# Kernel tuning notes

Hardware: AMD Instinct MI355X
Metric: run time of the kernel (lower is better)

Reference implementation:

```python
import jax, jax.numpy as jnp
import numpy as np

B, D, E, T, P = 65536, 256, 256, 128, 8  # batch, memory_dim, edge_feat_dim, time_dim, num_prototypes
LN_EPS = 1e-6
NORM_EPS = 1e-6


def _layer_norm(x, w, b):
    mu = jnp.mean(x, axis=-1, keepdims=True)
    var = jnp.mean(jnp.square(x - mu), axis=-1, keepdims=True)
    return (x - mu) / jnp.sqrt(var + LN_EPS) * w + b


def setup_inputs() -> dict:
    key = jax.random.key(0)
    ks = jax.random.split(key, 10)
    qin = D + E + T            # query_proj in_features
    gin = 2 * D + T            # gate_proj in_features
    return {
        "raw_memory": jax.random.normal(ks[0], (B, D), dtype=jnp.float32),
        "node_features": jax.random.normal(ks[1], (B, D), dtype=jnp.float32),
        "edge_features": jax.random.normal(ks[2], (B, E), dtype=jnp.float32),
        "time_encoding": jax.random.normal(ks[3], (B, T), dtype=jnp.float32),
        "prototypes": jax.random.normal(ks[4], (B, P, D), dtype=jnp.float32),
        # learned params (xavier gain=0.1 -> small)
        "Wq": jax.random.normal(ks[5], (D, qin), dtype=jnp.float32) * (0.1 * np.sqrt(2.0 / (D + qin))),
        "bq": jnp.zeros((D,), dtype=jnp.float32),
        "Wg": jax.random.normal(ks[6], (1, gin), dtype=jnp.float32) * (0.1 * np.sqrt(2.0 / (1 + gin))),
        "bg": jnp.zeros((1,), dtype=jnp.float32),
        "temperature": jnp.ones((1,), dtype=jnp.float32),
        "ln_w": jnp.ones((D,), dtype=jnp.float32),
        "ln_b": jnp.zeros((D,), dtype=jnp.float32),
    }


def reference(raw_memory, node_features, edge_features, time_encoding, prototypes,
              Wq, bq, Wg, bg, temperature, ln_w, ln_b):
    # query projection (inputs are finite so _sanitize_tensor is identity)
    q_in = jnp.concatenate([raw_memory, edge_features, time_encoding], axis=-1)  # [B, D+E+T]
    query = jnp.tanh(_layer_norm(q_in @ Wq.T + bq, ln_w, ln_b))                   # [B, D]

    # cosine similarity to per-node prototypes (F.normalize uses max(norm, eps))
    qn = query / jnp.maximum(jnp.linalg.norm(query, axis=-1, keepdims=True), NORM_EPS)
    pn = prototypes / jnp.maximum(jnp.linalg.norm(prototypes, axis=-1, keepdims=True), NORM_EPS)
    sim = jnp.clip(jnp.einsum('bd,bpd->bp', qn, pn), -10.0, 10.0)                 # [B, P]
    temp = jnp.clip(temperature, 0.5, 5.0)
    sim = sim / (temp + 0.01)

    attn = jnp.clip(jax.nn.softmax(sim, axis=-1), 0.0, 1.0)                       # [B, P]
    candidate = jnp.clip(jnp.einsum('bp,bpd->bd', attn, prototypes), -5.0, 5.0)   # [B, D]

    # gated update
    g_in = jnp.clip(jnp.concatenate([raw_memory, candidate, time_encoding], axis=-1), -50.0, 50.0)
    gate = jax.nn.sigmoid(jnp.clip(g_in @ Wg.T + bg, -10.0, 10.0))                # [B, 1]
    updated = (1.0 - gate) * raw_memory + gate * candidate
    updated = jnp.clip(_layer_norm(updated, ln_w, ln_b), -10.0, 10.0)
    return updated
```

## Files before the change

kernel.cpp:

```cpp
#include <hip/hip_runtime.h>
#include <cstdint>
#include <cstddef>

#define D 256
#define E 256
#define T 128
#define QIN 640
#define P 8
#define R 16
#define KP 648
#define DP 260

typedef __attribute__((ext_vector_type(8))) short bf16x8;
typedef __attribute__((ext_vector_type(4))) float f32x4;

__device__ __forceinline__ ushort f2bf(float f) {
  uint32_t u = __float_as_uint(f);
  u += 0x7fffu + ((u >> 16) & 1u);
  return (ushort)(u >> 16);
}

__device__ __forceinline__ float wsum(float v) {
#pragma unroll
  for (int o = 32; o > 0; o >>= 1) v += __shfl_xor(v, o, 64);
  return v;
}

__device__ __forceinline__ void wsum2(float& a, float& b) {
#pragma unroll
  for (int o = 32; o > 0; o >>= 1) {
    a += __shfl_xor(a, o, 64);
    b += __shfl_xor(b, o, 64);
  }
}

__device__ __forceinline__ float clampf(float x, float lo, float hi) {
  return fminf(fmaxf(x, lo), hi);
}

__global__ void prep_w2_kernel(const float* __restrict__ Wq, ushort* __restrict__ W2) {
  const int idx = blockIdx.x * 256 + threadIdx.x;
  const int n = idx / QIN;
  const int k = idx - n * QIN;
  W2[((((k >> 3) * D + n) << 3)) + (k & 7)] = f2bf(Wq[idx]);
}

template <bool PRE>
__global__ __launch_bounds__(256, 4) void fused_kernel(
    const float* __restrict__ raw, const float* __restrict__ edge,
    const float* __restrict__ tim, const float* __restrict__ proto,
    const float* __restrict__ Wq, const ushort* __restrict__ W2,
    const float* __restrict__ bq, const float* __restrict__ Wg,
    const float* __restrict__ bg, const float* __restrict__ temp,
    const float* __restrict__ lnw, const float* __restrict__ lnb,
    float* __restrict__ out) {
  __shared__ ushort qa[R][KP];
  __shared__ float qpre[R][DP];

  const int tid = threadIdx.x;
  const int r0 = blockIdx.x * R;

#pragma unroll
  for (int it = 0; it < (R * QIN / 4) / 256; ++it) {
    const int flat = it * 256 + tid;
    const int r = flat / (QIN / 4);
    const int p4 = (flat - r * (QIN / 4)) * 4;
    const size_t g = (size_t)(r0 + r);
    float4 v;
    if (p4 < D)          v = *(const float4*)(raw + g * D + p4);
    else if (p4 < D + E) v = *(const float4*)(edge + g * E + (p4 - D));
    else                 v = *(const float4*)(tim + g * T + (p4 - D - E));
    ushort4 h;
    h.x = f2bf(v.x); h.y = f2bf(v.y); h.z = f2bf(v.z); h.w = f2bf(v.w);
    *(ushort4*)&qa[r][p4] = h;
  }
  __syncthreads();

  const int w = tid >> 6;
  const int lane = tid & 63;
  const int lr = lane & 15;
  const int lh = lane >> 4;

  {
    f32x4 acc[4];
#pragma unroll
    for (int c = 0; c < 4; ++c) acc[c] = (f32x4){0.f, 0.f, 0.f, 0.f};

    for (int kb = 0; kb < QIN; kb += 32) {
      const bf16x8 af = *(const bf16x8*)&qa[lr][kb + lh * 8];
#pragma unroll
      for (int c = 0; c < 4; ++c) {
        const int n = w * 64 + c * 16 + lr;
        bf16x8 bfv;
        if (PRE) {
          bfv = *(const bf16x8*)&W2[(((kb >> 3) + lh) * D + n) << 3];
        } else {
          const float* src = Wq + (size_t)n * QIN + kb + lh * 8;
          const float4 a0 = *(const float4*)src;
          const float4 a1 = *(const float4*)(src + 4);
          bfv[0] = (short)f2bf(a0.x); bfv[1] = (short)f2bf(a0.y);
          bfv[2] = (short)f2bf(a0.z); bfv[3] = (short)f2bf(a0.w);
          bfv[4] = (short)f2bf(a1.x); bfv[5] = (short)f2bf(a1.y);
          bfv[6] = (short)f2bf(a1.z); bfv[7] = (short)f2bf(a1.w);
        }
        acc[c] = __builtin_amdgcn_mfma_f32_16x16x32_bf16(af, bfv, acc[c], 0, 0, 0);
      }
    }

#pragma unroll
    for (int c = 0; c < 4; ++c) {
      const int n = w * 64 + c * 16 + lr;
      const float bqv = bq[n];
#pragma unroll
      for (int i = 0; i < 4; ++i) qpre[lh * 4 + i][n] = acc[c][i] + bqv;
    }
  }
  __syncthreads();

  const float4 lnw4 = *(const float4*)(lnw + 4 * lane);
  const float4 lnb4 = *(const float4*)(lnb + 4 * lane);
  const float lw[4] = {lnw4.x, lnw4.y, lnw4.z, lnw4.w};
  const float lb[4] = {lnb4.x, lnb4.y, lnb4.z, lnb4.w};
  const float4 wga = *(const float4*)(Wg + 4 * lane);
  const float4 wgb = *(const float4*)(Wg + D + 4 * lane);
  const float2 wgt = *(const float2*)(Wg + 2 * D + 2 * lane);
  const float bgv = bg[0];
  const float invt = 1.0f / (clampf(temp[0], 0.5f, 5.0f) + 0.01f);

  for (int r = w; r < R; r += 4) {
    const size_t g = (size_t)(r0 + r);

    const float4 x4 = *(const float4*)&qpre[r][4 * lane];
    float x[4] = {x4.x, x4.y, x4.z, x4.w};
    float s = x[0] + x[1] + x[2] + x[3];
    const float mu = wsum(s) * (1.0f / 256.0f);
    float dx[4];
    float v = 0.f;
#pragma unroll
    for (int i = 0; i < 4; ++i) { dx[i] = x[i] - mu; v += dx[i] * dx[i]; }
    const float rstd = 1.0f / sqrtf(wsum(v) * (1.0f / 256.0f) + 1e-6f);
    float q[4];
    float qs = 0.f;
#pragma unroll
    for (int i = 0; i < 4; ++i) {
      q[i] = tanhf(dx[i] * rstd * lw[i] + lb[i]);
      qs += q[i] * q[i];
    }
    const float qdiv = fmaxf(sqrtf(wsum(qs)), 1e-6f);

    const float* pb = proto + (g * P) * D + 4 * lane;
    float pv[P][4];
    float sim[P];
#pragma unroll
    for (int p = 0; p < P; ++p) {
      const float4 p4 = *(const float4*)(pb + (size_t)p * D);
      pv[p][0] = p4.x; pv[p][1] = p4.y; pv[p][2] = p4.z; pv[p][3] = p4.w;
      float dt = q[0] * p4.x + q[1] * p4.y + q[2] * p4.z + q[3] * p4.w;
      float pn = p4.x * p4.x + p4.y * p4.y + p4.z * p4.z + p4.w * p4.w;
      wsum2(dt, pn);
      const float pdiv = fmaxf(sqrtf(pn), 1e-6f);
      sim[p] = clampf(dt / (qdiv * pdiv), -10.0f, 10.0f) * invt;
    }

    float m = sim[0];
#pragma unroll
    for (int p = 1; p < P; ++p) m = fmaxf(m, sim[p]);
    float es[P];
    float ssum = 0.f;
#pragma unroll
    for (int p = 0; p < P; ++p) { es[p] = expf(sim[p] - m); ssum += es[p]; }
    const float sinv = 1.0f / ssum;
    float cand[4] = {0.f, 0.f, 0.f, 0.f};
#pragma unroll
    for (int p = 0; p < P; ++p) {
      const float a = clampf(es[p] * sinv, 0.0f, 1.0f);
#pragma unroll
      for (int i = 0; i < 4; ++i) cand[i] = fmaf(a, pv[p][i], cand[i]);
    }
#pragma unroll
    for (int i = 0; i < 4; ++i) cand[i] = clampf(cand[i], -5.0f, 5.0f);

    const float4 raw4 = *(const float4*)(raw + g * D + 4 * lane);
    const float rr[4] = {raw4.x, raw4.y, raw4.z, raw4.w};
    const float2 t2 = *(const float2*)(tim + g * T + 2 * lane);
    float gsum =
        clampf(rr[0], -50.f, 50.f) * wga.x + clampf(rr[1], -50.f, 50.f) * wga.y +
        clampf(rr[2], -50.f, 50.f) * wga.z + clampf(rr[3], -50.f, 50.f) * wga.w +
        clampf(cand[0], -50.f, 50.f) * wgb.x + clampf(cand[1], -50.f, 50.f) * wgb.y +
        clampf(cand[2], -50.f, 50.f) * wgb.z + clampf(cand[3], -50.f, 50.f) * wgb.w +
        clampf(t2.x, -50.f, 50.f) * wgt.x + clampf(t2.y, -50.f, 50.f) * wgt.y;
    const float z = clampf(wsum(gsum) + bgv, -10.0f, 10.0f);
    const float gate = 1.0f / (1.0f + expf(-z));

    float upd[4];
    float s2 = 0.f;
#pragma unroll
    for (int i = 0; i < 4; ++i) {
      upd[i] = (1.0f - gate) * rr[i] + gate * cand[i];
      s2 += upd[i];
    }
    const float mu2 = wsum(s2) * (1.0f / 256.0f);
    float du[4];
    float v2 = 0.f;
#pragma unroll
    for (int i = 0; i < 4; ++i) { du[i] = upd[i] - mu2; v2 += du[i] * du[i]; }
    const float rstd2 = 1.0f / sqrtf(wsum(v2) * (1.0f / 256.0f) + 1e-6f);
    float4 y;
    y.x = clampf(du[0] * rstd2 * lw[0] + lb[0], -10.0f, 10.0f);
    y.y = clampf(du[1] * rstd2 * lw[1] + lb[1], -10.0f, 10.0f);
    y.z = clampf(du[2] * rstd2 * lw[2] + lb[2], -10.0f, 10.0f);
    y.w = clampf(du[3] * rstd2 * lw[3] + lb[3], -10.0f, 10.0f);
    *(float4*)(out + g * D + 4 * lane) = y;
  }
}

extern "C" void kernel_launch(void* const* d_in, const int* in_sizes, int n_in,
                              void* d_out, int out_size, void* d_ws, size_t ws_size,
                              hipStream_t stream) {
  const float* raw   = (const float*)d_in[0];
  const float* edge  = (const float*)d_in[2];
  const float* tim   = (const float*)d_in[3];
  const float* proto = (const float*)d_in[4];
  const float* Wq    = (const float*)d_in[5];
  const float* bq    = (const float*)d_in[6];
  const float* Wg    = (const float*)d_in[7];
  const float* bg    = (const float*)d_in[8];
  const float* temp  = (const float*)d_in[9];
  const float* lnw   = (const float*)d_in[10];
  const float* lnb   = (const float*)d_in[11];
  float* out = (float*)d_out;

  const int B = in_sizes[0] / D;
  const int nblk = B / R;

  const bool pre = ws_size >= (size_t)(QIN * D * sizeof(ushort));
  if (pre) {
    ushort* W2 = (ushort*)d_ws;
    prep_w2_kernel<<<(QIN * D) / 256, 256, 0, stream>>>(Wq, W2);
    fused_kernel<true><<<nblk, 256, 0, stream>>>(raw, edge, tim, proto, Wq, W2,
                                                 bq, Wg, bg, temp, lnw, lnb, out);
  } else {
    fused_kernel<false><<<nblk, 256, 0, stream>>>(raw, edge, tim, proto, Wq,
                                                  (const ushort*)nullptr, bq, Wg,
                                                  bg, temp, lnw, lnb, out);
  }
}
```

Baseline: 227.1 us.

## Map 16 lanes per row in epilogue and reload prototypes instead of holding them

The epilogue now handles four rows per wave at once: each row is split across 16 lanes holding 16 elements each, so reductions need only 4 shuffle steps and the serial per-row loop is gone. LayerNorm uses single-pass sum and sum-of-squares variance. Prototypes are read twice from global memory (once for similarity, once for the weighted sum), with an asm barrier on the pointer, to keep register pressure down rather than holding all 8×16 values. The risks are the extra prototype traffic, which is likely served from cache, and slightly different numerics from the one-pass variance.

```diff
diff --git a/kernel.cpp b/kernel.cpp
--- a/kernel.cpp
+++ b/kernel.cpp
@@ -20,15 +20,25 @@
   return (ushort)(u >> 16);
 }
 
-__device__ __forceinline__ float wsum(float v) {
-#pragma unroll
-  for (int o = 32; o > 0; o >>= 1) v += __shfl_xor(v, o, 64);
+__device__ __forceinline__ bf16x8 cvt8(const float* p) {
+  const float4 a = *(const float4*)p;
+  const float4 b = *(const float4*)(p + 4);
+  bf16x8 r;
+  r[0] = (short)f2bf(a.x); r[1] = (short)f2bf(a.y);
+  r[2] = (short)f2bf(a.z); r[3] = (short)f2bf(a.w);
+  r[4] = (short)f2bf(b.x); r[5] = (short)f2bf(b.y);
+  r[6] = (short)f2bf(b.z); r[7] = (short)f2bf(b.w);
+  return r;
+}
+
+__device__ __forceinline__ float rsum16(float v) {
+#pragma unroll
+  for (int o = 8; o > 0; o >>= 1) v += __shfl_xor(v, o, 64);
   return v;
 }
-
-__device__ __forceinline__ void wsum2(float& a, float& b) {
-#pragma unroll
-  for (int o = 32; o > 0; o >>= 1) {
+__device__ __forceinline__ void rsum16_2(float& a, float& b) {
+#pragma unroll
+  for (int o = 8; o > 0; o >>= 1) {
     a += __shfl_xor(a, o, 64);
     b += __shfl_xor(b, o, 64);
   }
@@ -91,22 +101,15 @@
 #pragma unroll
       for (int c = 0; c < 4; ++c) {
         const int n = w * 64 + c * 16 + lr;
-        bf16x8 bfv;
+        bf16x8 bv;
         if (PRE) {
-          bfv = *(const bf16x8*)&W2[(((kb >> 3) + lh) * D + n) << 3];
+          bv = *(const bf16x8*)&W2[(((kb >> 3) + lh) * D + n) << 3];
         } else {
-          const float* src = Wq + (size_t)n * QIN + kb + lh * 8;
-          const float4 a0 = *(const float4*)src;
-          const float4 a1 = *(const float4*)(src + 4);
-          bfv[0] = (short)f2bf(a0.x); bfv[1] = (short)f2bf(a0.y);
-          bfv[2] = (short)f2bf(a0.z); bfv[3] = (short)f2bf(a0.w);
-          bfv[4] = (short)f2bf(a1.x); bfv[5] = (short)f2bf(a1.y);
-          bfv[6] = (short)f2bf(a1.z); bfv[7] = (short)f2bf(a1.w);
+          bv = cvt8(Wq + (size_t)n * QIN + kb + lh * 8);
         }
-        acc[c] = __builtin_amdgcn_mfma_f32_16x16x32_bf16(af, bfv, acc[c], 0, 0, 0);
+        acc[c] = __builtin_amdgcn_mfma_f32_16x16x32_bf16(af, bv, acc[c], 0, 0, 0);
       }
     }
-
 #pragma unroll
     for (int c = 0; c < 4; ++c) {
       const int n = w * 64 + c * 16 + lr;
@@ -117,100 +120,151 @@
   }
   __syncthreads();
 
-  const float4 lnw4 = *(const float4*)(lnw + 4 * lane);
-  const float4 lnb4 = *(const float4*)(lnb + 4 * lane);
-  const float lw[4] = {lnw4.x, lnw4.y, lnw4.z, lnw4.w};
-  const float lb[4] = {lnb4.x, lnb4.y, lnb4.z, lnb4.w};
-  const float4 wga = *(const float4*)(Wg + 4 * lane);
-  const float4 wgb = *(const float4*)(Wg + D + 4 * lane);
-  const float2 wgt = *(const float2*)(Wg + 2 * D + 2 * lane);
+  const int rs = lane >> 4;
+  const int c16 = lane & 15;
+  const int r = w * 4 + rs;
+  const size_t g = (size_t)(r0 + r);
+  const int db = c16 * 16;
+
+  float rr[16];
+#pragma unroll
+  for (int c = 0; c < 4; ++c)
+    *(float4*)&rr[4 * c] = *(const float4*)(raw + g * D + db + 4 * c);
+  float t8[8];
+#pragma unroll
+  for (int c = 0; c < 2; ++c)
+    *(float4*)&t8[4 * c] = *(const float4*)(tim + g * T + c16 * 8 + 4 * c);
+
   const float bgv = bg[0];
   const float invt = 1.0f / (clampf(temp[0], 0.5f, 5.0f) + 0.01f);
 
-  for (int r = w; r < R; r += 4) {
-    const size_t g = (size_t)(r0 + r);
-
-    const float4 x4 = *(const float4*)&qpre[r][4 * lane];
-    float x[4] = {x4.x, x4.y, x4.z, x4.w};
-    float s = x[0] + x[1] + x[2] + x[3];
-    const float mu = wsum(s) * (1.0f / 256.0f);
-    float dx[4];
-    float v = 0.f;
-#pragma unroll
-    for (int i = 0; i < 4; ++i) { dx[i] = x[i] - mu; v += dx[i] * dx[i]; }
-    const float rstd = 1.0f / sqrtf(wsum(v) * (1.0f / 256.0f) + 1e-6f);
-    float q[4];
-    float qs = 0.f;
-#pragma unroll
-    for (int i = 0; i < 4; ++i) {
-      q[i] = tanhf(dx[i] * rstd * lw[i] + lb[i]);
-      qs += q[i] * q[i];
+  float x[16];
+#pragma unroll
+  for (int c = 0; c < 4; ++c)
+    *(float4*)&x[4 * c] = *(const float4*)&qpre[r][db + 4 * c];
+  float s = 0.f, ss = 0.f;
+#pragma unroll
+  for (int i = 0; i < 16; ++i) { s += x[i]; ss += x[i] * x[i]; }
+  rsum16_2(s, ss);
+  const float mu = s * (1.0f / 256.0f);
+  const float var = ss * (1.0f / 256.0f) - mu * mu;
+  const float rstd = 1.0f / sqrtf(var + 1e-6f);
+
+  float lwv[16], lbv[16];
+#pragma unroll
+  for (int c = 0; c < 4; ++c) {
+    *(float4*)&lwv[4 * c] = *(const float4*)(lnw + db + 4 * c);
+    *(float4*)&lbv[4 * c] = *(const float4*)(lnb + db + 4 * c);
+  }
+  float q[16];
+  float qs = 0.f;
+#pragma unroll
+  for (int i = 0; i < 16; ++i) {
+    q[i] = tanhf((x[i] - mu) * rstd * lwv[i] + lbv[i]);
+    qs += q[i] * q[i];
+  }
+  const float qdiv = fmaxf(sqrtf(rsum16(qs)), 1e-6f);
+
+  const float* pb = proto + g * (size_t)(P * D) + db;
+  float dt[8], pn[8];
+#pragma unroll
+  for (int p = 0; p < P; ++p) {
+    float pv[16];
+#pragma unroll
+    for (int c = 0; c < 4; ++c)
+      *(float4*)&pv[4 * c] = *(const float4*)(pb + (size_t)p * D + 4 * c);
+    float d = 0.f, n2 = 0.f;
+#pragma unroll
+    for (int i = 0; i < 16; ++i) { d += q[i] * pv[i]; n2 += pv[i] * pv[i]; }
+    dt[p] = d; pn[p] = n2;
+  }
+#pragma unroll
+  for (int o = 8; o > 0; o >>= 1) {
+#pragma unroll
+    for (int p = 0; p < P; ++p) {
+      dt[p] += __shfl_xor(dt[p], o, 64);
+      pn[p] += __shfl_xor(pn[p], o, 64);
     }
-    const float qdiv = fmaxf(sqrtf(wsum(qs)), 1e-6f);
-
-    const float* pb = proto + (g * P) * D + 4 * lane;
-    float pv[P][4];
-    float sim[P];
-#pragma unroll
-    for (int p = 0; p < P; ++p) {
-      const float4 p4 = *(const float4*)(pb + (size_t)p * D);
-      pv[p][0] = p4.x; pv[p][1] = p4.y; pv[p][2] = p4.z; pv[p][3] = p4.w;
-      float dt = q[0] * p4.x + q[1] * p4.y + q[2] * p4.z + q[3] * p4.w;
-      float pn = p4.x * p4.x + p4.y * p4.y + p4.z * p4.z + p4.w * p4.w;
-      wsum2(dt, pn);
-      const float pdiv = fmaxf(sqrtf(pn), 1e-6f);
-      sim[p] = clampf(dt / (qdiv * pdiv), -10.0f, 10.0f) * invt;
-    }
-
-    float m = sim[0];
-#pragma unroll
-    for (int p = 1; p < P; ++p) m = fmaxf(m, sim[p]);
-    float es[P];
-    float ssum = 0.f;
-#pragma unroll
-    for (int p = 0; p < P; ++p) { es[p] = expf(sim[p] - m); ssum += es[p]; }
-    const float sinv = 1.0f / ssum;
-    float cand[4] = {0.f, 0.f, 0.f, 0.f};
-#pragma unroll
-    for (int p = 0; p < P; ++p) {
-      const float a = clampf(es[p] * sinv, 0.0f, 1.0f);
-#pragma unroll
-      for (int i = 0; i < 4; ++i) cand[i] = fmaf(a, pv[p][i], cand[i]);
-    }
-#pragma unroll
-    for (int i = 0; i < 4; ++i) cand[i] = clampf(cand[i], -5.0f, 5.0f);
-
-    const float4 raw4 = *(const float4*)(raw + g * D + 4 * lane);
-    const float rr[4] = {raw4.x, raw4.y, raw4.z, raw4.w};
-    const float2 t2 = *(const float2*)(tim + g * T + 2 * lane);
-    float gsum =
-        clampf(rr[0], -50.f, 50.f) * wga.x + clampf(rr[1], -50.f, 50.f) * wga.y +
-        clampf(rr[2], -50.f, 50.f) * wga.z + clampf(rr[3], -50.f, 50.f) * wga.w +
-        clampf(cand[0], -50.f, 50.f) * wgb.x + clampf(cand[1], -50.f, 50.f) * wgb.y +
-        clampf(cand[2], -50.f, 50.f) * wgb.z + clampf(cand[3], -50.f, 50.f) * wgb.w +
-        clampf(t2.x, -50.f, 50.f) * wgt.x + clampf(t2.y, -50.f, 50.f) * wgt.y;
-    const float z = clampf(wsum(gsum) + bgv, -10.0f, 10.0f);
-    const float gate = 1.0f / (1.0f + expf(-z));
-
-    float upd[4];
-    float s2 = 0.f;
-#pragma unroll
-    for (int i = 0; i < 4; ++i) {
-      upd[i] = (1.0f - gate) * rr[i] + gate * cand[i];
-      s2 += upd[i];
-    }
-    const float mu2 = wsum(s2) * (1.0f / 256.0f);
-    float du[4];
-    float v2 = 0.f;
-#pragma unroll
-    for (int i = 0; i < 4; ++i) { du[i] = upd[i] - mu2; v2 += du[i] * du[i]; }
-    const float rstd2 = 1.0f / sqrtf(wsum(v2) * (1.0f / 256.0f) + 1e-6f);
+  }
+
+  float a[P];
+#pragma unroll
+  for (int p = 0; p < P; ++p) {
+    const float pdiv = fmaxf(sqrtf(pn[p]), 1e-6f);
+    a[p] = clampf(dt[p] / (qdiv * pdiv), -10.0f, 10.0f) * invt;
+  }
+  float m = a[0];
+#pragma unroll
+  for (int p = 1; p < P; ++p) m = fmaxf(m, a[p]);
+  float ssum = 0.f;
+#pragma unroll
+  for (int p = 0; p < P; ++p) { a[p] = expf(a[p] - m); ssum += a[p]; }
+  const float sinv = 1.0f / ssum;
+#pragma unroll
+  for (int p = 0; p < P; ++p) a[p] = clampf(a[p] * sinv, 0.0f, 1.0f);
+
+  uint64_t pbu = (uint64_t)pb;
+  asm volatile("" : "+v"(pbu));
+  const float* pb2 = (const float*)pbu;
+  float cd[16];
+#pragma unroll
+  for (int i = 0; i < 16; ++i) cd[i] = 0.f;
+#pragma unroll
+  for (int p = 0; p < P; ++p) {
+    float pv[16];
+#pragma unroll
+    for (int c = 0; c < 4; ++c)
+      *(float4*)&pv[4 * c] = *(const float4*)(pb2 + (size_t)p * D + 4 * c);
+#pragma unroll
+    for (int i = 0; i < 16; ++i) cd[i] = fmaf(a[p], pv[i], cd[i]);
+  }
+#pragma unroll
+  for (int i = 0; i < 16; ++i) cd[i] = clampf(cd[i], -5.0f, 5.0f);
+
+  float gsum = 0.f;
+#pragma unroll
+  for (int c = 0; c < 4; ++c) {
+    const float4 wr = *(const float4*)(Wg + db + 4 * c);
+    const float4 wc = *(const float4*)(Wg + D + db + 4 * c);
+    gsum += clampf(rr[4 * c + 0], -50.f, 50.f) * wr.x +
+            clampf(rr[4 * c + 1], -50.f, 50.f) * wr.y +
+            clampf(rr[4 * c + 2], -50.f, 50.f) * wr.z +
+            clampf(rr[4 * c + 3], -50.f, 50.f) * wr.w;
+    gsum += clampf(cd[4 * c + 0], -50.f, 50.f) * wc.x +
+            clampf(cd[4 * c + 1], -50.f, 50.f) * wc.y +
+            clampf(cd[4 * c + 2], -50.f, 50.f) * wc.z +
+            clampf(cd[4 * c + 3], -50.f, 50.f) * wc.w;
+  }
+#pragma unroll
+  for (int c = 0; c < 2; ++c) {
+    const float4 wt = *(const float4*)(Wg + 2 * D + c16 * 8 + 4 * c);
+    gsum += clampf(t8[4 * c + 0], -50.f, 50.f) * wt.x +
+            clampf(t8[4 * c + 1], -50.f, 50.f) * wt.y +
+            clampf(t8[4 * c + 2], -50.f, 50.f) * wt.z +
+            clampf(t8[4 * c + 3], -50.f, 50.f) * wt.w;
+  }
+  const float z = clampf(rsum16(gsum) + bgv, -10.0f, 10.0f);
+  const float gate = 1.0f / (1.0f + expf(-z));
+
+  float upd[16];
+  float s2 = 0.f, ss2 = 0.f;
+#pragma unroll
+  for (int i = 0; i < 16; ++i) {
+    upd[i] = (1.0f - gate) * rr[i] + gate * cd[i];
+    s2 += upd[i]; ss2 += upd[i] * upd[i];
+  }
+  rsum16_2(s2, ss2);
+  const float mu2 = s2 * (1.0f / 256.0f);
+  const float var2 = ss2 * (1.0f / 256.0f) - mu2 * mu2;
+  const float rstd2 = 1.0f / sqrtf(var2 + 1e-6f);
+#pragma unroll
+  for (int c = 0; c < 4; ++c) {
     float4 y;
-    y.x = clampf(du[0] * rstd2 * lw[0] + lb[0], -10.0f, 10.0f);
-    y.y = clampf(du[1] * rstd2 * lw[1] + lb[1], -10.0f, 10.0f);
-    y.z = clampf(du[2] * rstd2 * lw[2] + lb[2], -10.0f, 10.0f);
-    y.w = clampf(du[3] * rstd2 * lw[3] + lb[3], -10.0f, 10.0f);
-    *(float4*)(out + g * D + 4 * lane) = y;
+    y.x = clampf((upd[4 * c + 0] - mu2) * rstd2 * lwv[4 * c + 0] + lbv[4 * c + 0], -10.0f, 10.0f);
+    y.y = clampf((upd[4 * c + 1] - mu2) * rstd2 * lwv[4 * c + 1] + lbv[4 * c + 1], -10.0f, 10.0f);
+    y.z = clampf((upd[4 * c + 2] - mu2) * rstd2 * lwv[4 * c + 2] + lbv[4 * c + 2], -10.0f, 10.0f);
+    y.w = clampf((upd[4 * c + 3] - mu2) * rstd2 * lwv[4 * c + 3] + lbv[4 * c + 3], -10.0f, 10.0f);
+    *(float4*)(out + g * D + db + 4 * c) = y;
   }
 }
 
@@ -233,8 +287,7 @@
   const int B = in_sizes[0] / D;
   const int nblk = B / R;
 
-  const bool pre = ws_size >= (size_t)(QIN * D * sizeof(ushort));
-  if (pre) {
+  if (ws_size >= (size_t)QIN * D * sizeof(ushort)) {
     ushort* W2 = (ushort*)d_ws;
     prep_w2_kernel<<<(QIN * D) / 256, 256, 0, stream>>>(Wq, W2);
     fused_kernel<true><<<nblk, 256, 0, stream>>>(raw, edge, tim, proto, Wq, W2,
```

Measured after the change: 300.4 us. +32.2%, slower.
